# Performance work log

Hardware: AMD Instinct MI355X
Metric: run time of the kernel (lower is better)

Reference implementation:

```python
import jax, jax.numpy as jnp
import numpy as np

B, N, F, H, E, L = 4, 4096, 256, 256, 262144, 3
NTOT = B * N
EPS = 1e-5
NEG_SLOPE = 0.2  # PyG GATConv default leaky_relu slope


def setup_inputs() -> dict:
    key = jax.random.key(0)
    ks = jax.random.split(key, 10)
    s = 0.05
    return {
        "x": jax.random.normal(ks[0], (B, 1, N, F), jnp.float32),
        "edge_index": jax.random.randint(ks[1], (2, E), 0, NTOT, jnp.int64),
        "tc_w": jax.random.normal(ks[2], (H, F, 3), jnp.float32) * s,   # Conv1d weight [out,in,k]
        "tc_b": jax.random.normal(ks[3], (H,), jnp.float32) * s,
        "gat_W": jax.random.normal(ks[4], (L, H, H), jnp.float32) * s,  # per-layer lin weight (in==hidden)
        "gat_as": jax.random.normal(ks[5], (L, H), jnp.float32) * s,    # att_src
        "gat_ad": jax.random.normal(ks[6], (L, H), jnp.float32) * s,    # att_dst
        "gat_b": jax.random.normal(ks[7], (L, H), jnp.float32) * s,
        "ln_g": jnp.ones((H,), jnp.float32),
        "ln_b": jnp.zeros((H,), jnp.float32),
    }


def _gat_layer(h, W, a_s, a_d, b, src, dst):
    # h: [NTOT, H]; heads=1, eval mode (no dropout), self-loops already in src/dst
    hw = h @ W                                  # [NTOT, H]
    e = jax.nn.leaky_relu((hw @ a_s)[src] + (hw @ a_d)[dst], NEG_SLOPE)  # [E']
    m = jax.ops.segment_max(e, dst, num_segments=NTOT)
    ex = jnp.exp(e - m[dst])
    denom = jax.ops.segment_sum(ex, dst, num_segments=NTOT)
    alpha = ex / denom[dst]                     # edge softmax over incoming edges
    out = jax.ops.segment_sum(alpha[:, None] * hw[src], dst, num_segments=NTOT)
    return out + b


def reference(x, edge_index, tc_w, tc_b, gat_W, gat_as, gat_ad, gat_b, ln_g, ln_b):
    # add self loops (PyG GATConv default add_self_loops=True)
    loops = jnp.arange(NTOT, dtype=edge_index.dtype)
    src = jnp.concatenate([edge_index[0], loops])
    dst = jnp.concatenate([edge_index[1], loops])

    def conv1d(y):  # y: [B, C, N]
        o = jax.lax.conv_general_dilated(y, tc_w, (1,), [(1, 1)],
                                         dimension_numbers=("NCH", "OIH", "NCH"))
        return o + tc_b[None, :, None]

    xt = jnp.transpose(x[:, 0], (0, 2, 1))      # [B, F, N]
    xt = jax.nn.relu(conv1d(xt) + xt)           # temporal conv + residual

    h = jnp.transpose(xt, (0, 2, 1)).reshape(NTOT, H)
    for l in range(L):
        h = jax.nn.relu(_gat_layer(h, gat_W[l], gat_as[l], gat_ad[l], gat_b[l], src, dst))

    hg = jnp.transpose(h.reshape(B, N, H), (0, 2, 1))  # [B, H, N]
    out = conv1d(hg)[:, :, 0]                   # [B, H]

    mu = jnp.mean(out, axis=-1, keepdims=True)
    var = jnp.var(out, axis=-1, keepdims=True)
    out = (out - mu) / jnp.sqrt(var + EPS) * ln_g + ln_b
    return jax.nn.relu(out)
```

## Files before the change

### kernel.cpp

```cpp
#include <hip/hip_runtime.h>
#include <hip/hip_bf16.h>
#include <math.h>

#define NTOT 16384
#define HDIM 256
#define BBATCH 4
#define NSEQ 4096
#define FDIM 256
#define NE 262144
#define NEE (NE + NTOT)
#define NLAYER 3
#define LN_EPS 1e-5f
#define SLOPE 0.2f
#define CAP 64

typedef __attribute__((ext_vector_type(8))) short bf16x8;
typedef __attribute__((ext_vector_type(4))) float f32x4;

#define LDW 80
#define SLDW 72

#define OFF_HA   0u
#define OFF_HW   8388608u
#define OFF_WC   16777216u
#define OFF_WL   17170432u
#define OFF_SP   17563648u
#define OFF_DP   17825792u
#define OFF_CNT  18087936u
#define OFF_CSR  18153472u
#define OFF_WT   22347776u
#define OFF_F1   23134208u
#define OFF_F2   23199744u
#define OFF_L1   23265280u
#define OFF_L2   23330816u
#define OFF_CT   23396352u

static __device__ __forceinline__ unsigned short f2b(float f) {
    __hip_bfloat16 h = __float2bfloat16(f);
    return __builtin_bit_cast(unsigned short, h);
}
static __device__ __forceinline__ float b2f(unsigned short u) {
    __hip_bfloat16 h = __builtin_bit_cast(__hip_bfloat16, u);
    return __bfloat162float(h);
}
static __device__ __forceinline__ float rlanef(float v, int l) {
    return __builtin_bit_cast(float, __builtin_amdgcn_readlane(__builtin_bit_cast(int, v), l));
}

static __device__ __forceinline__ void wave_append(bool isNew, int src, int lane,
                                                   int* ctp, int* list) {
    unsigned long long mask = __ballot(isNew);
    int base = 0;
    if (lane == 0 && mask) base = atomicAdd(ctp, (int)__popcll(mask));
    base = __shfl(base, 0);
    if (isNew) {
        int off = (int)__popcll(mask & ((1ull << lane) - 1ull));
        list[base + off] = src;
    }
}

__global__ __launch_bounds__(256) void k_pre(const float* __restrict__ tcw, const float* __restrict__ gatW,
                                             unsigned short* __restrict__ wcB, unsigned short* __restrict__ WTb,
                                             float* __restrict__ wT, int* __restrict__ cnt,
                                             int* __restrict__ flag1, int* __restrict__ flag2,
                                             int* __restrict__ ct) {
    int b = blockIdx.x, t = threadIdx.x;
    if (b < 256) {
        const float* s = tcw + b * 768 + t * 3;
        wcB[b * 768 + 0 + t]   = f2b(s[0]);
        wcB[b * 768 + 256 + t] = f2b(s[1]);
        wcB[b * 768 + 512 + t] = f2b(s[2]);
    } else if (b < 1024) {
        int ln = b - 256; int n = ln & 255; int l = ln >> 8;
        WTb[(size_t)l * 65536 + n * 256 + t] = f2b(gatW[(size_t)l * 65536 + t * 256 + n]);
    } else if (b < 1792) {
        int fk = b - 1024; int f = fk / 3, k = fk - 3 * f;
        wT[(k * FDIM + f) * HDIM + t] = tcw[t * 768 + fk];
    } else if (b < 1808) {
        int i = ((b - 1792) * 256 + t) * 4;
        *(int4*)(cnt + i) = make_int4(0, 0, 0, 0);
    } else if (b < 1824) {
        int i = ((b - 1808) * 256 + t) * 4;
        *(int4*)(flag1 + i) = make_int4(0, 0, 0, 0);
    } else if (b < 1840) {
        int i = ((b - 1824) * 256 + t) * 4;
        *(int4*)(flag2 + i) = make_int4(0, 0, 0, 0);
    } else {
        if (t < 2) ct[t] = 0;
    }
}

__global__ __launch_bounds__(256) void k_conv(const float* __restrict__ x,
                                              const unsigned short* __restrict__ wcB,
                                              const float* __restrict__ tcb,
                                              unsigned short* __restrict__ hAb,
                                              const int* __restrict__ ei, int* __restrict__ cnt,
                                              int* __restrict__ csr,
                                              int* __restrict__ flag2, int* __restrict__ list2,
                                              int* __restrict__ ct) {
    __shared__ char slab[130 * SLDW];
    __shared__ char Bs[3 * 64 * LDW];
    int t = threadIdx.x;
    if (blockIdx.x >= 128) {
        int cid = (blockIdx.x - 128) * 4 + blockIdx.y;
        int e = cid * 256 + t;
        int src, dst;
        if (e < NE) { src = ei[e]; dst = ei[NE + e]; } else { src = dst = e - NE; }
        int slot = atomicAdd(&cnt[dst], 1);
        if (slot < CAP) csr[dst * CAP + slot] = src;
        bool isNew = false;
        if ((dst & 4095) < 2) isNew = (atomicExch(&flag2[src], 1) == 0);
        wave_append(isNew, src, t & 63, &ct[0], list2);
        return;
    }
    int m0 = blockIdx.x * 128, n0 = blockIdx.y * 64;
    int bb = m0 >> 12;
    int nloc0 = m0 & 4095;
    int w = t >> 6, lane = t & 63;
    int wr = w >> 1, wc = w & 1;
    int row16 = lane & 15, kg = lane >> 4;
    int rA = t >> 1, hh = t & 1;
    f32x4 acc[4][2];
    #pragma unroll
    for (int mi = 0; mi < 4; ++mi)
        #pragma unroll
        for (int ni = 0; ni < 2; ++ni) acc[mi][ni] = (f32x4)(0.f);

    for (int kb = 0; kb < 8; ++kb) {
        int c0 = kb * 32;
        __syncthreads();
        {
            int nl = nloc0 - 1 + rA;
            ushort4 o0 = make_ushort4(0,0,0,0), o1 = make_ushort4(0,0,0,0),
                    o2 = make_ushort4(0,0,0,0), o3 = make_ushort4(0,0,0,0);
            if ((unsigned)nl < 4096u) {
                const float4* s = (const float4*)(x + ((size_t)(bb << 12) + nl) * 256 + c0 + hh * 16);
                float4 f0 = s[0], f1 = s[1], f2 = s[2], f3 = s[3];
                o0 = make_ushort4(f2b(f0.x), f2b(f0.y), f2b(f0.z), f2b(f0.w));
                o1 = make_ushort4(f2b(f1.x), f2b(f1.y), f2b(f1.z), f2b(f1.w));
                o2 = make_ushort4(f2b(f2.x), f2b(f2.y), f2b(f2.z), f2b(f2.w));
                o3 = make_ushort4(f2b(f3.x), f2b(f3.y), f2b(f3.z), f2b(f3.w));
            }
            char* dstp = &slab[rA * SLDW + hh * 32];
            *(ushort4*)(dstp)      = o0;
            *(ushort4*)(dstp + 8)  = o1;
            *(ushort4*)(dstp + 16) = o2;
            *(ushort4*)(dstp + 24) = o3;
        }
        if (t < 16) {
            int r = 128 + (t >> 3), u = t & 7;
            int nl = nloc0 - 1 + r;
            ushort4 o = make_ushort4(0,0,0,0);
            if ((unsigned)nl < 4096u) {
                const float4* s = (const float4*)(x + ((size_t)(bb << 12) + nl) * 256 + c0 + u * 4);
                float4 f = s[0];
                o = make_ushort4(f2b(f.x), f2b(f.y), f2b(f.z), f2b(f.w));
            }
            *(ushort4*)&slab[r * SLDW + u * 8] = o;
        }
        {
            int rB = t >> 2, u = t & 3;
            const unsigned short* wrow = wcB + (size_t)(n0 + rB) * 768 + c0 + u * 8;
            #pragma unroll
            for (int p = 0; p < 3; ++p)
                *(uint4*)&Bs[p * 64 * LDW + rB * LDW + u * 16] = *(const uint4*)(wrow + p * 256);
        }
        __syncthreads();
        #pragma unroll
        for (int p = 0; p < 3; ++p) {
            bf16x8 bfr[2];
            #pragma unroll
            for (int ni = 0; ni < 2; ++ni)
                bfr[ni] = *(bf16x8*)&Bs[p * 64 * LDW + (wc * 32 + ni * 16 + row16) * LDW + kg * 16];
            #pragma unroll
            for (int mi = 0; mi < 4; ++mi) {
                bf16x8 afr = *(bf16x8*)&slab[(wr * 64 + mi * 16 + row16 + p) * SLDW + kg * 16];
                acc[mi][0] = __builtin_amdgcn_mfma_f32_16x16x32_bf16(afr, bfr[0], acc[mi][0], 0, 0, 0);
                acc[mi][1] = __builtin_amdgcn_mfma_f32_16x16x32_bf16(afr, bfr[1], acc[mi][1], 0, 0, 0);
            }
        }
    }
    #pragma unroll
    for (int mi = 0; mi < 4; ++mi)
        #pragma unroll
        for (int ni = 0; ni < 2; ++ni) {
            int rowl = wr * 64 + mi * 16 + kg * 4;
            int coll = wc * 32 + ni * 16 + row16;
            int n = n0 + coll;
            float bc = tcb[n];
            #pragma unroll
            for (int q = 0; q < 4; ++q) {
                size_t node = (size_t)(m0 + rowl + q);
                float v = acc[mi][ni][q] + bc + x[node * 256 + n];
                v = v > 0.f ? v : 0.f;
                hAb[node * 256 + n] = f2b(v);
            }
        }
}

__global__ __launch_bounds__(256) void k_gemm_layer(const unsigned short* __restrict__ hAb,
                                                    const unsigned short* __restrict__ WT,
                                                    const float* __restrict__ as, const float* __restrict__ ad,
                                                    unsigned short* __restrict__ hwB,
                                                    float* __restrict__ sPart, float* __restrict__ dPart,
                                                    const int* __restrict__ cnt, const int* __restrict__ csr,
                                                    int* __restrict__ flag1,
                                                    int* __restrict__ list1, const int* __restrict__ list2,
                                                    int* __restrict__ ct) {
    __shared__ char lds[128 * LDW + 64 * LDW];
    __shared__ float sRed[256], dRed[256];
    char* As = lds;
    char* Bs = lds + 128 * LDW;
    int t = threadIdx.x;
    if (blockIdx.x == 128) {
        int lane = t & 63;
        int n2 = ct[0];
        int total = n2 * CAP;
        for (int p = blockIdx.y * 256 + t; p < total; p += 1024) {
            int node = list2[p >> 6];
            int j = p & (CAP - 1);
            int src = 0; bool isNew = false;
            if (j < cnt[node]) {
                src = csr[node * CAP + j];
                isNew = (atomicExch(&flag1[src], 1) == 0);
            }
            wave_append(isNew, src, lane, &ct[1], list1);
        }
        return;
    }
    int m0 = blockIdx.x * 128, n0 = blockIdx.y * 64;
    int w = t >> 6, lane = t & 63;
    int wr = w >> 1, wc = w & 1;
    int row16 = lane & 15, kg = lane >> 4;
    int rA = t >> 1, hh = t & 1;
    f32x4 acc[4][2];
    #pragma unroll
    for (int mi = 0; mi < 4; ++mi)
        #pragma unroll
        for (int ni = 0; ni < 2; ++ni) acc[mi][ni] = (f32x4)(0.f);

    for (int kb = 0; kb < 256; kb += 32) {
        {
            const uint4* src = (const uint4*)(hAb + (size_t)(m0 + rA) * 256 + kb + hh * 16);
            uint4 v0 = src[0], v1 = src[1];
            *(uint4*)&As[rA * LDW + hh * 32] = v0;
            *(uint4*)&As[rA * LDW + hh * 32 + 16] = v1;
        }
        if (t < 128) {
            int rB = t >> 1;
            const uint4* src = (const uint4*)(WT + (size_t)(n0 + rB) * 256 + kb + hh * 16);
            uint4 v0 = src[0], v1 = src[1];
            *(uint4*)&Bs[rB * LDW + hh * 32] = v0;
            *(uint4*)&Bs[rB * LDW + hh * 32 + 16] = v1;
        }
        __syncthreads();
        bf16x8 bfr[2];
        #pragma unroll
        for (int ni = 0; ni < 2; ++ni)
            bfr[ni] = *(bf16x8*)&Bs[(wc * 32 + ni * 16 + row16) * LDW + kg * 16];
        #pragma unroll
        for (int mi = 0; mi < 4; ++mi) {
            bf16x8 afr = *(bf16x8*)&As[(wr * 64 + mi * 16 + row16) * LDW + kg * 16];
            acc[mi][0] = __builtin_amdgcn_mfma_f32_16x16x32_bf16(afr, bfr[0], acc[mi][0], 0, 0, 0);
            acc[mi][1] = __builtin_amdgcn_mfma_f32_16x16x32_bf16(afr, bfr[1], acc[mi][1], 0, 0, 0);
        }
        __syncthreads();
    }
    #pragma unroll
    for (int mi = 0; mi < 4; ++mi)
        #pragma unroll
        for (int ni = 0; ni < 2; ++ni) {
            int rowl = wr * 64 + mi * 16 + kg * 4;
            int coll = wc * 32 + ni * 16 + row16;
            size_t base = (size_t)(m0 + rowl) * 256 + n0 + coll;
            #pragma unroll
            for (int q = 0; q < 4; ++q) hwB[base + (size_t)q * 256] = f2b(acc[mi][ni][q]);
        }
    float asv0 = as[n0 + wc * 32 + row16];
    float asv1 = as[n0 + wc * 32 + 16 + row16];
    float adv0 = ad[n0 + wc * 32 + row16];
    float adv1 = ad[n0 + wc * 32 + 16 + row16];
    #pragma unroll
    for (int mi = 0; mi < 4; ++mi)
        #pragma unroll
        for (int q = 0; q < 4; ++q) {
            float ps = acc[mi][0][q] * asv0 + acc[mi][1][q] * asv1;
            float pd = acc[mi][0][q] * adv0 + acc[mi][1][q] * adv1;
            #pragma unroll
            for (int o = 1; o < 16; o <<= 1) { ps += __shfl_xor(ps, o); pd += __shfl_xor(pd, o); }
            if (row16 == 0) {
                int rowl = wr * 64 + mi * 16 + kg * 4 + q;
                sRed[rowl * 2 + wc] = ps;
                dRed[rowl * 2 + wc] = pd;
            }
        }
    __syncthreads();
    if (t < 128) {
        sPart[(size_t)blockIdx.y * NTOT + m0 + t] = sRed[t * 2] + sRed[t * 2 + 1];
        dPart[(size_t)blockIdx.y * NTOT + m0 + t] = dRed[t * 2] + dRed[t * 2 + 1];
    }
}

__global__ __launch_bounds__(256) void k_gemm_list(const unsigned short* __restrict__ hAb,
                                                   const unsigned short* __restrict__ WT,
                                                   const float* __restrict__ as, const float* __restrict__ ad,
                                                   unsigned short* __restrict__ hwB,
                                                   float* __restrict__ sPart, float* __restrict__ dPart,
                                                   const int* __restrict__ list, const int* __restrict__ cptr) {
    __shared__ char lds[128 * LDW + 64 * LDW];
    __shared__ float sRed[256], dRed[256];
    __shared__ int rows[128];
    char* As = lds;
    char* Bs = lds + 128 * LDW;
    int t = threadIdx.x;
    int n = *cptr;
    int m0 = blockIdx.x * 128;
    if (m0 >= n) return;
    int n0 = blockIdx.y * 64;
    if (t < 128) {
        int idx = m0 + t;
        rows[t] = list[idx < n ? idx : n - 1];
    }
    __syncthreads();
    int w = t >> 6, lane = t & 63;
    int wr = w >> 1, wc = w & 1;
    int row16 = lane & 15, kg = lane >> 4;
    int rA = t >> 1, hh = t & 1;
    f32x4 acc[4][2];
    #pragma unroll
    for (int mi = 0; mi < 4; ++mi)
        #pragma unroll
        for (int ni = 0; ni < 2; ++ni) acc[mi][ni] = (f32x4)(0.f);

    for (int kb = 0; kb < 256; kb += 32) {
        {
            const uint4* src = (const uint4*)(hAb + (size_t)rows[rA] * 256 + kb + hh * 16);
            uint4 v0 = src[0], v1 = src[1];
            *(uint4*)&As[rA * LDW + hh * 32] = v0;
            *(uint4*)&As[rA * LDW + hh * 32 + 16] = v1;
        }
        if (t < 128) {
            int rB = t >> 1;
            const uint4* src = (const uint4*)(WT + (size_t)(n0 + rB) * 256 + kb + hh * 16);
            uint4 v0 = src[0], v1 = src[1];
            *(uint4*)&Bs[rB * LDW + hh * 32] = v0;
            *(uint4*)&Bs[rB * LDW + hh * 32 + 16] = v1;
        }
        __syncthreads();
        bf16x8 bfr[2];
        #pragma unroll
        for (int ni = 0; ni < 2; ++ni)
            bfr[ni] = *(bf16x8*)&Bs[(wc * 32 + ni * 16 + row16) * LDW + kg * 16];
        #pragma unroll
        for (int mi = 0; mi < 4; ++mi) {
            bf16x8 afr = *(bf16x8*)&As[(wr * 64 + mi * 16 + row16) * LDW + kg * 16];
            acc[mi][0] = __builtin_amdgcn_mfma_f32_16x16x32_bf16(afr, bfr[0], acc[mi][0], 0, 0, 0);
            acc[mi][1] = __builtin_amdgcn_mfma_f32_16x16x32_bf16(afr, bfr[1], acc[mi][1], 0, 0, 0);
        }
        __syncthreads();
    }
    #pragma unroll
    for (int mi = 0; mi < 4; ++mi)
        #pragma unroll
        for (int ni = 0; ni < 2; ++ni) {
            int rowl = wr * 64 + mi * 16 + kg * 4;
            int coll = wc * 32 + ni * 16 + row16;
            #pragma unroll
            for (int q = 0; q < 4; ++q)
                hwB[(size_t)rows[rowl + q] * 256 + n0 + coll] = f2b(acc[mi][ni][q]);
        }
    float asv0 = as[n0 + wc * 32 + row16];
    float asv1 = as[n0 + wc * 32 + 16 + row16];
    float adv0 = ad[n0 + wc * 32 + row16];
    float adv1 = ad[n0 + wc * 32 + 16 + row16];
    #pragma unroll
    for (int mi = 0; mi < 4; ++mi)
        #pragma unroll
        for (int q = 0; q < 4; ++q) {
            float ps = acc[mi][0][q] * asv0 + acc[mi][1][q] * asv1;
            float pd = acc[mi][0][q] * adv0 + acc[mi][1][q] * adv1;
            #pragma unroll
            for (int o = 1; o < 16; o <<= 1) { ps += __shfl_xor(ps, o); pd += __shfl_xor(pd, o); }
            if (row16 == 0) {
                int rowl = wr * 64 + mi * 16 + kg * 4 + q;
                sRed[rowl * 2 + wc] = ps;
                dRed[rowl * 2 + wc] = pd;
            }
        }
    __syncthreads();
    if (t < 128) {
        int node = rows[t];
        sPart[(size_t)blockIdx.y * NTOT + node] = sRed[t * 2] + sRed[t * 2 + 1];
        dPart[(size_t)blockIdx.y * NTOT + node] = dRed[t * 2] + dRed[t * 2 + 1];
    }
}

__global__ __launch_bounds__(256) void k_agg_list(const unsigned short* __restrict__ hwB,
                                                  const float* __restrict__ sPart, const float* __restrict__ dPart,
                                                  const int* __restrict__ cnt, const int* __restrict__ csr,
                                                  const float* __restrict__ bias,
                                                  unsigned short* __restrict__ hout,
                                                  const int* __restrict__ list, const int* __restrict__ cptr) {
    int tid = threadIdx.x;
    int wave = tid >> 6, lane = tid & 63;
    int n = *cptr;
    const ushort4* hw4 = (const ushort4*)hwB;
    for (int idx = blockIdx.x * 4 + wave; idx < n; idx += gridDim.x * 4) {
        int node = list[idx];
        int deg = cnt[node];
        const int* bucket = csr + node * CAP;
        float di = dPart[node] + dPart[NTOT + node] + dPart[2 * NTOT + node] + dPart[3 * NTOT + node];
        float denom = 0.f;
        float a0 = 0.f, a1 = 0.f, a2 = 0.f, a3 = 0.f;
        for (int cb = 0; cb < deg; cb += 64) {
            int j = cb + lane;
            int sj = 0;
            float myw = 0.f;
            if (j < deg) {
                sj = bucket[j];
                float sv = sPart[sj] + sPart[NTOT + sj] + sPart[2 * NTOT + sj] + sPart[3 * NTOT + sj];
                float e = sv + di;
                e = e > 0.f ? e : SLOPE * e;
                myw = __expf(e);
            }
            float csum = myw;
            #pragma unroll
            for (int o = 1; o < 64; o <<= 1) csum += __shfl_xor(csum, o);
            denom += csum;
            int c = deg - cb; if (c > 64) c = 64;
            int q = 0;
            for (; q + 8 <= c; q += 8) {
                int si[8]; float wi[8]; ushort4 vv[8];
                #pragma unroll
                for (int u = 0; u < 8; ++u) {
                    si[u] = __builtin_amdgcn_readlane(sj, q + u);
                    wi[u] = rlanef(myw, q + u);
                }
                #pragma unroll
                for (int u = 0; u < 8; ++u) vv[u] = hw4[(size_t)si[u] * 64 + lane];
                #pragma unroll
                for (int u = 0; u < 8; ++u) {
                    a0 = fmaf(wi[u], b2f(vv[u].x), a0);
                    a1 = fmaf(wi[u], b2f(vv[u].y), a1);
                    a2 = fmaf(wi[u], b2f(vv[u].z), a2);
                    a3 = fmaf(wi[u], b2f(vv[u].w), a3);
                }
            }
            if (q < c) {
                int rem = c - q;
                int si[8]; float wi[8]; ushort4 vv[8];
                #pragma unroll
                for (int u = 0; u < 8; ++u) {
                    int qq = q + (u < rem ? u : 0);
                    si[u] = __builtin_amdgcn_readlane(sj, qq);
                    wi[u] = (u < rem) ? rlanef(myw, qq) : 0.f;
                }
                #pragma unroll
                for (int u = 0; u < 8; ++u) vv[u] = hw4[(size_t)si[u] * 64 + lane];
                #pragma unroll
                for (int u = 0; u < 8; ++u) {
                    a0 = fmaf(wi[u], b2f(vv[u].x), a0);
                    a1 = fmaf(wi[u], b2f(vv[u].y), a1);
                    a2 = fmaf(wi[u], b2f(vv[u].z), a2);
                    a3 = fmaf(wi[u], b2f(vv[u].w), a3);
                }
            }
        }
        float inv = 1.f / denom;
        float4 bb = ((const float4*)bias)[lane];
        ushort4 o;
        float o0 = a0 * inv + bb.x; o.x = f2b(o0 > 0.f ? o0 : 0.f);
        float o1 = a1 * inv + bb.y; o.y = f2b(o1 > 0.f ? o1 : 0.f);
        float o2 = a2 * inv + bb.z; o.z = f2b(o2 > 0.f ? o2 : 0.f);
        float o3 = a3 * inv + bb.w; o.w = f2b(o3 > 0.f ? o3 : 0.f);
        ((ushort4*)hout)[(size_t)node * 64 + lane] = o;
    }
}

__global__ __launch_bounds__(256) void k_aggfinal(const unsigned short* __restrict__ hwB,
                                                  const float* __restrict__ sPart, const float* __restrict__ dPart,
                                                  const int* __restrict__ cnt, const int* __restrict__ csr,
                                                  const float* __restrict__ bias,
                                                  const float* __restrict__ wT, const float* __restrict__ tcb,
                                                  const float* __restrict__ g, const float* __restrict__ bln,
                                                  float* __restrict__ out) {
    __shared__ float r01[2][HDIM];
    __shared__ float red[16];
    int b = blockIdx.x, t = threadIdx.x;
    int w = t >> 6, lane = t & 63;
    if (w < 2) {
        int node = b * NSEQ + w;
        int deg = cnt[node];
        const int* bucket = csr + node * CAP;
        float di = dPart[node] + dPart[NTOT + node] + dPart[2 * NTOT + node] + dPart[3 * NTOT + node];
        const ushort4* hw4 = (const ushort4*)hwB;
        float denom = 0.f;
        float a0 = 0.f, a1 = 0.f, a2 = 0.f, a3 = 0.f;
        for (int cb = 0; cb < deg; cb += 64) {
            int j = cb + lane;
            int sj = 0;
            float myw = 0.f;
            if (j < deg) {
                sj = bucket[j];
                float sv = sPart[sj] + sPart[NTOT + sj] + sPart[2 * NTOT + sj] + sPart[3 * NTOT + sj];
                float e = sv + di;
                e = e > 0.f ? e : SLOPE * e;
                myw = __expf(e);
            }
            float csum = myw;
            #pragma unroll
            for (int o = 1; o < 64; o <<= 1) csum += __shfl_xor(csum, o);
            denom += csum;
            int c = deg - cb; if (c > 64) c = 64;
            for (int q = 0; q < c; ++q) {
                int sq = __builtin_amdgcn_readlane(sj, q);
                float wq = rlanef(myw, q);
                ushort4 v = hw4[(size_t)sq * 64 + lane];
                a0 = fmaf(wq, b2f(v.x), a0); a1 = fmaf(wq, b2f(v.y), a1);
                a2 = fmaf(wq, b2f(v.z), a2); a3 = fmaf(wq, b2f(v.w), a3);
            }
        }
        float inv = 1.f / denom;
        float4 bb = ((const float4*)bias)[lane];
        float o0 = a0 * inv + bb.x;
        float o1 = a1 * inv + bb.y;
        float o2 = a2 * inv + bb.z;
        float o3 = a3 * inv + bb.w;
        r01[w][lane * 4 + 0] = o0 > 0.f ? o0 : 0.f;
        r01[w][lane * 4 + 1] = o1 > 0.f ? o1 : 0.f;
        r01[w][lane * 4 + 2] = o2 > 0.f ? o2 : 0.f;
        r01[w][lane * 4 + 3] = o3 > 0.f ? o3 : 0.f;
    }
    __syncthreads();
    int c = t;
    float a = tcb[c];
    for (int f = 0; f < FDIM; ++f) {
        a = fmaf(wT[(1 * FDIM + f) * HDIM + c], r01[0][f], a);
        a = fmaf(wT[(2 * FDIM + f) * HDIM + c], r01[1][f], a);
    }
    float ss = a, sq = a * a;
    #pragma unroll
    for (int o = 1; o < 64; o <<= 1) { ss += __shfl_xor(ss, o); sq += __shfl_xor(sq, o); }
    if (lane == 0) { red[w] = ss; red[8 + w] = sq; }
    __syncthreads();
    float tot = 0.f, totq = 0.f;
    #pragma unroll
    for (int u = 0; u < 4; ++u) { tot += red[u]; totq += red[8 + u]; }
    float mu = tot * (1.f / HDIM);
    float var = totq * (1.f / HDIM) - mu * mu;
    float v = (a - mu) * rsqrtf(var + LN_EPS) * g[c] + bln[c];
    out[b * HDIM + c] = v > 0.f ? v : 0.f;
}

extern "C" void kernel_launch(void* const* d_in, const int* in_sizes, int n_in,
                              void* d_out, int out_size, void* d_ws, size_t ws_size,
                              hipStream_t stream) {
    const float* x     = (const float*)d_in[0];
    const int*   ei    = (const int*)d_in[1];
    const float* tcw   = (const float*)d_in[2];
    const float* tcb   = (const float*)d_in[3];
    const float* gatW  = (const float*)d_in[4];
    const float* gatas = (const float*)d_in[5];
    const float* gatad = (const float*)d_in[6];
    const float* gatb  = (const float*)d_in[7];
    const float* lng   = (const float*)d_in[8];
    const float* lnb   = (const float*)d_in[9];
    float* out = (float*)d_out;

    char* ws = (char*)d_ws;
    unsigned short* hAb = (unsigned short*)(ws + OFF_HA);
    unsigned short* hwB = (unsigned short*)(ws + OFF_HW);
    unsigned short* wcB = (unsigned short*)(ws + OFF_WC);
    unsigned short* WTb = (unsigned short*)(ws + OFF_WL);
    float* sPart = (float*)(ws + OFF_SP);
    float* dPart = (float*)(ws + OFF_DP);
    int*   cnt  = (int*)(ws + OFF_CNT);
    int*   csr  = (int*)(ws + OFF_CSR);
    float* wT   = (float*)(ws + OFF_WT);
    int*   flag1 = (int*)(ws + OFF_F1);
    int*   flag2 = (int*)(ws + OFF_F2);
    int*   list1 = (int*)(ws + OFF_L1);
    int*   list2 = (int*)(ws + OFF_L2);
    int*   ct    = (int*)(ws + OFF_CT);

    k_pre<<<1841, 256, 0, stream>>>(tcw, gatW, wcB, WTb, wT, cnt, flag1, flag2, ct);
    k_conv<<<dim3(128 + 272, 4), 256, 0, stream>>>(x, wcB, tcb, hAb, ei, cnt, csr,
                                                   flag2, list2, ct);

    k_gemm_layer<<<dim3(129, 4), 256, 0, stream>>>(
        hAb, WTb, gatas, gatad, hwB, sPart, dPart,
        cnt, csr, flag1, list1, list2, ct);
    k_agg_list<<<1024, 256, 0, stream>>>(hwB, sPart, dPart, cnt, csr, gatb, hAb, list1, ct + 1);

    k_gemm_list<<<dim3(128, 4), 256, 0, stream>>>(
        hAb, WTb + 65536, gatas + HDIM, gatad + HDIM, hwB, sPart, dPart, list1, ct + 1);
    k_agg_list<<<128, 256, 0, stream>>>(hwB, sPart, dPart, cnt, csr, gatb + HDIM, hAb, list2, ct);

    k_gemm_list<<<dim3(4, 4), 256, 0, stream>>>(
        hAb, WTb + 131072, gatas + 2 * HDIM, gatad + 2 * HDIM, hwB, sPart, dPart, list2, ct);
    k_aggfinal<<<BBATCH, 256, 0, stream>>>(hwB, sPart, dPart, cnt, csr, gatb + 2 * HDIM,
                                           wT, tcb, lng, lnb, out);
}
```

Before: 117.5 us.

## Fuse last-layer GEMM into final aggregation kernel per batch

Replaces the last-layer list GEMM launch and the final aggregation kernel with one kernel per batch. That kernel gathers the neighbour rows of the two needed nodes, runs the 128-row MFMA GEMM itself, and computes the attention source/destination scores in shared memory before doing the softmax aggregation and the closing conv/LayerNorm. This removes a kernel launch and the global round-trip of the partial score arrays. In exchange each of only 4 blocks does all four column tiles serially. Degrees are clamped to CAP and each node is assumed to have at most 64 neighbours in one chunk.

Measured after the change: 135.7 us. 15.5% more time.

```diff
diff --git a/kernel.cpp b/kernel.cpp
--- a/kernel.cpp
+++ b/kernel.cpp
@@ -9,7 +9,6 @@
 #define FDIM 256
 #define NE 262144
 #define NEE (NE + NTOT)
-#define NLAYER 3
 #define LN_EPS 1e-5f
 #define SLOPE 0.2f
 #define CAP 64
@@ -477,48 +476,134 @@
     }
 }
 
-__global__ __launch_bounds__(256) void k_aggfinal(const unsigned short* __restrict__ hwB,
-                                                  const float* __restrict__ sPart, const float* __restrict__ dPart,
-                                                  const int* __restrict__ cnt, const int* __restrict__ csr,
-                                                  const float* __restrict__ bias,
-                                                  const float* __restrict__ wT, const float* __restrict__ tcb,
-                                                  const float* __restrict__ g, const float* __restrict__ bln,
-                                                  float* __restrict__ out) {
+__global__ __launch_bounds__(256) void k_final3(const unsigned short* __restrict__ hAb,
+                                                const unsigned short* __restrict__ WT,
+                                                const float* __restrict__ as, const float* __restrict__ ad,
+                                                unsigned short* __restrict__ hwB,
+                                                const int* __restrict__ cnt, const int* __restrict__ csr,
+                                                const float* __restrict__ bias,
+                                                const float* __restrict__ wT, const float* __restrict__ tcb,
+                                                const float* __restrict__ g, const float* __restrict__ bln,
+                                                float* __restrict__ out) {
+    __shared__ char As[128 * LDW];
+    __shared__ char Bs[64 * LDW];
+    __shared__ float sRed[256], dRed[256];
+    __shared__ int rows[128];
+    __shared__ float sLoc[128], dLoc[128];
     __shared__ float r01[2][HDIM];
     __shared__ float red[16];
+    __shared__ int selfSlot[2];
     int b = blockIdx.x, t = threadIdx.x;
     int w = t >> 6, lane = t & 63;
+
+    int node0 = b * NSEQ, node1 = node0 + 1;
+    int c0 = cnt[node0]; int deg0 = c0 < CAP ? c0 : CAP;
+    int c1 = cnt[node1]; int deg1 = c1 < CAP ? c1 : CAP;
+    if (t < 128) {
+        int which = t >> 6, j = t & 63;
+        int nd = which ? node1 : node0;
+        int dg = which ? deg1 : deg0;
+        int src = csr[nd * CAP + (j < dg ? j : 0)];
+        rows[t] = src;
+        if (src == nd && j < dg) selfSlot[which] = t;
+        sLoc[t] = 0.f; dLoc[t] = 0.f;
+    }
+    __syncthreads();
+
+    int wr = w >> 1, wc = w & 1;
+    int row16 = lane & 15, kg = lane >> 4;
+    int rA = t >> 1, hh = t & 1;
+    for (int cb4 = 0; cb4 < 4; ++cb4) {
+        int n0 = cb4 * 64;
+        f32x4 acc[4][2];
+        #pragma unroll
+        for (int mi = 0; mi < 4; ++mi)
+            #pragma unroll
+            for (int ni = 0; ni < 2; ++ni) acc[mi][ni] = (f32x4)(0.f);
+        for (int kb = 0; kb < 256; kb += 32) {
+            __syncthreads();
+            {
+                const uint4* src = (const uint4*)(hAb + (size_t)rows[rA] * 256 + kb + hh * 16);
+                uint4 v0 = src[0], v1 = src[1];
+                *(uint4*)&As[rA * LDW + hh * 32] = v0;
+                *(uint4*)&As[rA * LDW + hh * 32 + 16] = v1;
+            }
+            if (t < 128) {
+                int rB = t >> 1;
+                const uint4* src = (const uint4*)(WT + (size_t)(n0 + rB) * 256 + kb + hh * 16);
+                uint4 v0 = src[0], v1 = src[1];
+                *(uint4*)&Bs[rB * LDW + hh * 32] = v0;
+                *(uint4*)&Bs[rB * LDW + hh * 32 + 16] = v1;
+            }
+            __syncthreads();
+            bf16x8 bfr[2];
+            #pragma unroll
+            for (int ni = 0; ni < 2; ++ni)
+                bfr[ni] = *(bf16x8*)&Bs[(wc * 32 + ni * 16 + row16) * LDW + kg * 16];
+            #pragma unroll
+            for (int mi = 0; mi < 4; ++mi) {
+                bf16x8 afr = *(bf16x8*)&As[(wr * 64 + mi * 16 + row16) * LDW + kg * 16];
+                acc[mi][0] = __builtin_amdgcn_mfma_f32_16x16x32_bf16(afr, bfr[0], acc[mi][0], 0, 0, 0);
+                acc[mi][1] = __builtin_amdgcn_mfma_f32_16x16x32_bf16(afr, bfr[1], acc[mi][1], 0, 0, 0);
+            }
+        }
+        #pragma unroll
+        for (int mi = 0; mi < 4; ++mi)
+            #pragma unroll
+            for (int ni = 0; ni < 2; ++ni) {
+                int rowl = wr * 64 + mi * 16 + kg * 4;
+                int coll = wc * 32 + ni * 16 + row16;
+                #pragma unroll
+                for (int q = 0; q < 4; ++q)
+                    hwB[(size_t)rows[rowl + q] * 256 + n0 + coll] = f2b(acc[mi][ni][q]);
+            }
+        float asv0 = as[n0 + wc * 32 + row16];
+        float asv1 = as[n0 + wc * 32 + 16 + row16];
+        float adv0 = ad[n0 + wc * 32 + row16];
+        float adv1 = ad[n0 + wc * 32 + 16 + row16];
+        #pragma unroll
+        for (int mi = 0; mi < 4; ++mi)
+            #pragma unroll
+            for (int q = 0; q < 4; ++q) {
+                float ps = acc[mi][0][q] * asv0 + acc[mi][1][q] * asv1;
+                float pd = acc[mi][0][q] * adv0 + acc[mi][1][q] * adv1;
+                #pragma unroll
+                for (int o = 1; o < 16; o <<= 1) { ps += __shfl_xor(ps, o); pd += __shfl_xor(pd, o); }
+                if (row16 == 0) {
+                    int rowl = wr * 64 + mi * 16 + kg * 4 + q;
+                    sRed[rowl * 2 + wc] = ps;
+                    dRed[rowl * 2 + wc] = pd;
+                }
+            }
+        __syncthreads();
+        if (t < 128) {
+            sLoc[t] += sRed[t * 2] + sRed[t * 2 + 1];
+            dLoc[t] += dRed[t * 2] + dRed[t * 2 + 1];
+        }
+        __syncthreads();
+    }
+
     if (w < 2) {
-        int node = b * NSEQ + w;
-        int deg = cnt[node];
-        const int* bucket = csr + node * CAP;
-        float di = dPart[node] + dPart[NTOT + node] + dPart[2 * NTOT + node] + dPart[3 * NTOT + node];
+        int dg = w ? deg1 : deg0;
+        float di = dLoc[selfSlot[w]];
+        float myw = 0.f;
+        int row = w * 64 + lane;
+        if (lane < dg) {
+            float e = sLoc[row] + di;
+            e = e > 0.f ? e : SLOPE * e;
+            myw = __expf(e);
+        }
+        float denom = myw;
+        #pragma unroll
+        for (int o = 1; o < 64; o <<= 1) denom += __shfl_xor(denom, o);
+        float a0 = 0.f, a1 = 0.f, a2 = 0.f, a3 = 0.f;
         const ushort4* hw4 = (const ushort4*)hwB;
-        float denom = 0.f;
-        float a0 = 0.f, a1 = 0.f, a2 = 0.f, a3 = 0.f;
-        for (int cb = 0; cb < deg; cb += 64) {
-            int j = cb + lane;
-            int sj = 0;
-            float myw = 0.f;
-            if (j < deg) {
-                sj = bucket[j];
-                float sv = sPart[sj] + sPart[NTOT + sj] + sPart[2 * NTOT + sj] + sPart[3 * NTOT + sj];
-                float e = sv + di;
-                e = e > 0.f ? e : SLOPE * e;
-                myw = __expf(e);
-            }
-            float csum = myw;
-            #pragma unroll
-            for (int o = 1; o < 64; o <<= 1) csum += __shfl_xor(csum, o);
-            denom += csum;
-            int c = deg - cb; if (c > 64) c = 64;
-            for (int q = 0; q < c; ++q) {
-                int sq = __builtin_amdgcn_readlane(sj, q);
-                float wq = rlanef(myw, q);
-                ushort4 v = hw4[(size_t)sq * 64 + lane];
-                a0 = fmaf(wq, b2f(v.x), a0); a1 = fmaf(wq, b2f(v.y), a1);
-                a2 = fmaf(wq, b2f(v.z), a2); a3 = fmaf(wq, b2f(v.w), a3);
-            }
+        for (int q = 0; q < dg; ++q) {
+            int sq = rows[w * 64 + q];
+            float wq = rlanef(myw, q);
+            ushort4 v = hw4[(size_t)sq * 64 + lane];
+            a0 = fmaf(wq, b2f(v.x), a0); a1 = fmaf(wq, b2f(v.y), a1);
+            a2 = fmaf(wq, b2f(v.z), a2); a3 = fmaf(wq, b2f(v.w), a3);
         }
         float inv = 1.f / denom;
         float4 bb = ((const float4*)bias)[lane];
@@ -596,8 +681,6 @@
         hAb, WTb + 65536, gatas + HDIM, gatad + HDIM, hwB, sPart, dPart, list1, ct + 1);
     k_agg_list<<<128, 256, 0, stream>>>(hwB, sPart, dPart, cnt, csr, gatb + HDIM, hAb, list2, ct);
 
-    k_gemm_list<<<dim3(4, 4), 256, 0, stream>>>(
-        hAb, WTb + 131072, gatas + 2 * HDIM, gatad + 2 * HDIM, hwB, sPart, dPart, list2, ct);
-    k_aggfinal<<<BBATCH, 256, 0, stream>>>(hwB, sPart, dPart, cnt, csr, gatb + 2 * HDIM,
-                                           wT, tcb, lng, lnb, out);
-}
+    k_final3<<<BBATCH, 256, 0, stream>>>(hAb, WTb + 131072, gatas + 2 * HDIM, gatad + 2 * HDIM,
+                                         hwB, cnt, csr, gatb + 2 * HDIM, wT, tcb, lng, lnb, out);
+}
```
